# Optimization experiments

Measured on AMD Instinct MI355X. Metric: run time of the kernel, lower is better.

## Reference

```python
import jax, jax.numpy as jnp
import numpy as np

IN_C = 256
OUT_C = 256
HID = IN_C * 2
N_POINTS = 262144
N_NODES = 8192
B = 16
MAX_NODES = 512
EPS = 1e-5


def _mlp(h, w1, b1, g1, be1, w2, b2):
    # PyG MLP([C, 2C, out], norm='layer_norm'): lin -> layernorm -> relu -> (dropout, eval=identity) -> lin
    h = h @ w1 + b1
    mu = jnp.mean(h, axis=-1, keepdims=True)
    var = jnp.var(h, axis=-1, keepdims=True)
    h = (h - mu) * jax.lax.rsqrt(var + EPS) * g1 + be1
    h = jax.nn.relu(h)
    return h @ w2 + b2


def setup_inputs() -> dict:
    key = jax.random.key(0)
    ks = jax.random.split(key, 16)
    x = jax.random.normal(ks[0], (N_POINTS, IN_C), dtype=jnp.float32)
    f_point_batches = jnp.sort(jax.random.randint(ks[1], (N_POINTS,), 0, N_NODES)).astype(jnp.int32)
    # equal-sized graphs (16 graphs x 512 nodes), sorted as torch.split/pad_sequence assume
    g_node_batches = jnp.repeat(jnp.arange(B, dtype=jnp.int32), MAX_NODES)
    s = 1.0 / np.sqrt(IN_C)
    s2 = 1.0 / np.sqrt(HID)
    def lin(k, fan_in, shape, scale):
        return jax.random.uniform(k, shape, jnp.float32, -scale, scale)
    params = {}
    for i, name in enumerate(['Wq', 'Wk']):
        base = 2 + i * 6
        params[f'{name}_w1'] = lin(ks[base + 0], IN_C, (IN_C, HID), s)
        params[f'{name}_b1'] = lin(ks[base + 1], IN_C, (HID,), s)
        params[f'{name}_g1'] = jnp.ones((HID,), jnp.float32)
        params[f'{name}_be1'] = jnp.zeros((HID,), jnp.float32)
        params[f'{name}_w2'] = lin(ks[base + 2], HID, (HID, OUT_C), s2)
        params[f'{name}_b2'] = lin(ks[base + 3], HID, (OUT_C,), s2)
    return dict(x=x, f_point_batches=f_point_batches, g_node_batches=g_node_batches,
                num_graphs=B, max_nodes=MAX_NODES, **params)


def reference(x, f_point_batches, g_node_batches, num_graphs, max_nodes,
              Wq_w1, Wq_b1, Wq_g1, Wq_be1, Wq_w2, Wq_b2,
              Wk_w1, Wk_b1, Wk_g1, Wk_be1, Wk_w2, Wk_b2):
    n_nodes = g_node_batches.shape[0]
    C = x.shape[1]
    # scatter_mean over points -> per-node feature means [n_nodes, C]
    sums = jax.ops.segment_sum(x, f_point_batches, num_segments=n_nodes)
    cnt = jax.ops.segment_sum(jnp.ones((x.shape[0],), x.dtype), f_point_batches, num_segments=n_nodes)
    mean = sums / jnp.maximum(cnt, 1.0)[:, None]
    # ragged split by graph + pad_sequence -> [B, max_nodes, C]
    starts = jnp.searchsorted(g_node_batches, jnp.arange(num_graphs, dtype=g_node_batches.dtype))
    pos = jnp.arange(n_nodes) - starts[g_node_batches]
    padded = jnp.zeros((num_graphs, max_nodes, C), x.dtype).at[g_node_batches, pos].set(mean, mode='drop')
    q = _mlp(padded, Wq_w1, Wq_b1, Wq_g1, Wq_be1, Wq_w2, Wq_b2)  # [B, MAXN, out]
    k = _mlp(padded, Wk_w1, Wk_b1, Wk_g1, Wk_be1, Wk_w2, Wk_b2)
    return jnp.einsum('bnd,bmd->bnm', q, k)  # bmm(q, k^T)
```

## Files before the change

kernel.cpp:

```cpp
#include <hip/hip_runtime.h>
#include <hip/hip_bf16.h>

#define N_POINTS 262144
#define N_NODES  8192
#define IN_C     256
#define HID      512
#define OUT_C    256
#define NB       16
#define MAXN     512
#define EPSV     1e-5f
#define NPB      32

typedef __attribute__((ext_vector_type(8))) short short8;
typedef __attribute__((ext_vector_type(4))) float f32x4;
#define MFMA16(a, b, c) __builtin_amdgcn_mfma_f32_16x16x32_bf16((a), (b), (c), 0, 0, 0)


__global__ __launch_bounds__(256) void prelude_k(
    const int* __restrict__ fpb, int* __restrict__ starts,
    const float* __restrict__ W1q, const float* __restrict__ W1k,
    const float* __restrict__ W2q, const float* __restrict__ W2k,
    __hip_bfloat16* __restrict__ P1q, __hip_bfloat16* __restrict__ P1k,
    __hip_bfloat16* __restrict__ P2q, __hip_bfloat16* __restrict__ P2k)
{
  if (blockIdx.x < 1024) {
    const int i = blockIdx.x * 256 + threadIdx.x;
    const int cur = fpb[i];
    const int prev = (i == 0) ? -1 : fpb[i - 1];
    for (int n = prev + 1; n <= cur; ++n) starts[n] = i;
    if (i == N_POINTS - 1)
      for (int n = cur + 1; n <= N_NODES; ++n) starts[n] = N_POINTS;
    return;
  }
  const int bid = blockIdx.x - 1024;
  const int sel = bid >> 6;
  const float* W; __hip_bfloat16* P; int N;
  switch (sel) {
    case 0:  W = W1q; P = P1q; N = HID;   break;
    case 1:  W = W1k; P = P1k; N = HID;   break;
    case 2:  W = W2q; P = P2q; N = OUT_C; break;
    default: W = W2k; P = P2k; N = OUT_C; break;
  }
  const int idx = (bid & 63) * 256 + threadIdx.x;
  const int NF = N >> 4;
  const int lane = idx & 63;
  const int nf = (idx >> 6) % NF;
  const int ks = idx / (64 * NF);
  const int k0 = ks * 32 + (lane >> 4) * 8;
  const int n  = nf * 16 + (lane & 15);
  __hip_bfloat16 tmp[8];
  #pragma unroll
  for (int j = 0; j < 8; ++j) tmp[j] = __float2bfloat16(W[(size_t)(k0 + j) * N + n]);
  *(uint4*)(P + (size_t)idx * 8) = *(uint4*)tmp;
}

__global__ __launch_bounds__(256) void scatter_mean_k(
    const float* __restrict__ x, const int* __restrict__ starts,
    __hip_bfloat16* __restrict__ mean)
{
  const int node = blockIdx.x;
  const int start = starts[node];
  const int end   = starts[node + 1];
  const int t  = threadIdx.x;
  const int c4 = t & 63;
  const int rr = t >> 6;

  float4 s0 = make_float4(0.f, 0.f, 0.f, 0.f);
  float4 s1 = make_float4(0.f, 0.f, 0.f, 0.f);
  int r = start + rr;
  for (; r + 8 <= end; r += 8) {
    float4 v0 = *(const float4*)(x + (size_t)r * IN_C + c4 * 4);
    float4 v1 = *(const float4*)(x + (size_t)(r + 4) * IN_C + c4 * 4);
    s0.x += v0.x; s0.y += v0.y; s0.z += v0.z; s0.w += v0.w;
    s1.x += v1.x; s1.y += v1.y; s1.z += v1.z; s1.w += v1.w;
  }
  for (; r < end; r += 4) {
    float4 v = *(const float4*)(x + (size_t)r * IN_C + c4 * 4);
    s0.x += v.x; s0.y += v.y; s0.z += v.z; s0.w += v.w;
  }
  s0.x += s1.x; s0.y += s1.y; s0.z += s1.z; s0.w += s1.w;

  __shared__ float4 red[256];
  red[t] = s0;
  __syncthreads();
  if (t < 64) {
    float4 a = red[t], b = red[t + 64], c = red[t + 128], d = red[t + 192];
    const int cnt = end - start;
    const float inv = cnt > 0 ? 1.0f / (float)cnt : 0.0f;
    __hip_bfloat16 o[4];
    o[0] = __float2bfloat16((a.x + b.x + c.x + d.x) * inv);
    o[1] = __float2bfloat16((a.y + b.y + c.y + d.y) * inv);
    o[2] = __float2bfloat16((a.z + b.z + c.z + d.z) * inv);
    o[3] = __float2bfloat16((a.w + b.w + c.w + d.w) * inv);
    *(uint2*)(mean + (size_t)node * IN_C + t * 4) = *(uint2*)o;
  }
}

__global__ __launch_bounds__(512, 2) void mlp_fused_k(
    const __hip_bfloat16* __restrict__ mean,
    const __hip_bfloat16* __restrict__ P1q, const __hip_bfloat16* __restrict__ P2q,
    const float* __restrict__ b1q, const float* __restrict__ g1q,
    const float* __restrict__ be1q, const float* __restrict__ b2q,
    const __hip_bfloat16* __restrict__ P1k, const __hip_bfloat16* __restrict__ P2k,
    const float* __restrict__ b1k, const float* __restrict__ g1k,
    const float* __restrict__ be1k, const float* __restrict__ b2k,
    __hip_bfloat16* __restrict__ qo, __hip_bfloat16* __restrict__ ko)
{
  const int n0 = blockIdx.x * NPB;
  const int t = threadIdx.x;
  const int w = t >> 6, l = t & 63, lg = l >> 4, lm = l & 15;
  const int h = w >> 2;
  const int c = w & 3;

  const __hip_bfloat16* P1 = h ? P1k : P1q;
  const __hip_bfloat16* P2 = h ? P2k : P2q;
  const float* b1  = h ? b1k  : b1q;
  const float* g1  = h ? g1k  : g1q;
  const float* be1 = h ? be1k : be1q;
  const float* b2  = h ? b2k  : b2q;
  __hip_bfloat16* out = h ? ko : qo;

  __shared__ __hip_bfloat16 As[NPB * 264];
  __shared__ __hip_bfloat16 Hs[2][NPB * 520];
  __shared__ float lnp[8][NPB][2];

  #pragma unroll
  for (int it = 0; it < 2; ++it) {
    const int idx = t + it * 512;
    const int r = idx >> 5, c8 = idx & 31;
    uint4 v = *(const uint4*)(mean + (size_t)(n0 + r) * IN_C + c8 * 8);
    *(uint4*)(As + r * 264 + c8 * 8) = v;
  }
  __syncthreads();

  f32x4 acc1[2][8];
  #pragma unroll
  for (int mi = 0; mi < 2; ++mi)
    #pragma unroll
    for (int nj = 0; nj < 8; ++nj)
      #pragma unroll
      for (int r = 0; r < 4; ++r) acc1[mi][nj][r] = 0.f;

  for (int ks = 0; ks < 8; ++ks) {
    short8 a0 = *(const short8*)(As + lm * 264 + ks * 32 + lg * 8);
    short8 a1 = *(const short8*)(As + (16 + lm) * 264 + ks * 32 + lg * 8);
    const __hip_bfloat16* bp = P1 + ((size_t)(ks * 32 + c * 8) * 64 + l) * 8;
    #pragma unroll
    for (int nj = 0; nj < 8; ++nj) {
      short8 b = *(const short8*)(bp + (size_t)nj * 512);
      acc1[0][nj] = MFMA16(a0, b, acc1[0][nj]);
      acc1[1][nj] = MFMA16(a1, b, acc1[1][nj]);
    }
  }

  float b1v[8], g1v[8], e1v[8];
  #pragma unroll
  for (int nj = 0; nj < 8; ++nj) {
    const int col = c * 128 + nj * 16 + lm;
    b1v[nj] = b1[col]; g1v[nj] = g1[col]; e1v[nj] = be1[col];
  }
  #pragma unroll
  for (int mi = 0; mi < 2; ++mi)
    #pragma unroll
    for (int nj = 0; nj < 8; ++nj)
      #pragma unroll
      for (int r = 0; r < 4; ++r) acc1[mi][nj][r] += b1v[nj];

  #pragma unroll
  for (int mi = 0; mi < 2; ++mi)
    #pragma unroll
    for (int r = 0; r < 4; ++r) {
      float s = 0.f, q = 0.f;
      #pragma unroll
      for (int nj = 0; nj < 8; ++nj) {
        const float v = acc1[mi][nj][r];
        s += v; q += v * v;
      }
      #pragma unroll
      for (int off = 1; off < 16; off <<= 1) {
        s += __shfl_xor(s, off);
        q += __shfl_xor(q, off);
      }
      if (lm == 0) {
        const int row = mi * 16 + lg * 4 + r;
        lnp[w][row][0] = s;
        lnp[w][row][1] = q;
      }
    }
  __syncthreads();

  #pragma unroll
  for (int mi = 0; mi < 2; ++mi)
    #pragma unroll
    for (int r = 0; r < 4; ++r) {
      const int row = mi * 16 + lg * 4 + r;
      float S = 0.f, Q = 0.f;
      #pragma unroll
      for (int w2 = 0; w2 < 4; ++w2) {
        S += lnp[h * 4 + w2][row][0];
        Q += lnp[h * 4 + w2][row][1];
      }
      const float mu = S * (1.0f / HID);
      const float rs = rsqrtf(Q * (1.0f / HID) - mu * mu + EPSV);
      #pragma unroll
      for (int nj = 0; nj < 8; ++nj) {
        const float y = (acc1[mi][nj][r] - mu) * rs * g1v[nj] + e1v[nj];
        Hs[h][row * 520 + c * 128 + nj * 16 + lm] = __float2bfloat16(fmaxf(y, 0.f));
      }
    }
  __syncthreads();

  f32x4 acc2[2][4];
  #pragma unroll
  for (int mi = 0; mi < 2; ++mi)
    #pragma unroll
    for (int nj = 0; nj < 4; ++nj)
      #pragma unroll
      for (int r = 0; r < 4; ++r) acc2[mi][nj][r] = 0.f;

  for (int ks = 0; ks < 16; ++ks) {
    short8 a0 = *(const short8*)(Hs[h] + lm * 520 + ks * 32 + lg * 8);
    short8 a1 = *(const short8*)(Hs[h] + (16 + lm) * 520 + ks * 32 + lg * 8);
    const __hip_bfloat16* bp = P2 + ((size_t)(ks * 16 + c * 4) * 64 + l) * 8;
    #pragma unroll
    for (int nj = 0; nj < 4; ++nj) {
      short8 b = *(const short8*)(bp + (size_t)nj * 512);
      acc2[0][nj] = MFMA16(a0, b, acc2[0][nj]);
      acc2[1][nj] = MFMA16(a1, b, acc2[1][nj]);
    }
  }

  float b2v[4];
  #pragma unroll
  for (int nj = 0; nj < 4; ++nj) b2v[nj] = b2[c * 64 + nj * 16 + lm];
  #pragma unroll
  for (int mi = 0; mi < 2; ++mi)
    #pragma unroll
    for (int nj = 0; nj < 4; ++nj)
      #pragma unroll
      for (int r = 0; r < 4; ++r) {
        const int row = n0 + mi * 16 + lg * 4 + r;
        const int col = c * 64 + nj * 16 + lm;
        out[(size_t)row * OUT_C + col] = __float2bfloat16(acc2[mi][nj][r] + b2v[nj]);
      }
}

__global__ __launch_bounds__(256, 4) void bmm_k(
    const __hip_bfloat16* __restrict__ q, const __hip_bfloat16* __restrict__ k,
    float* __restrict__ out)
{
  const int b  = blockIdx.z;
  const int n0 = blockIdx.x * 64;
  const int m0 = blockIdx.y * 64;
  const int t = threadIdx.x;
  const int w = t >> 6, l = t & 63, lg = l >> 4, lm = l & 15;

  const __hip_bfloat16* qb = q + ((size_t)b * MAXN + n0 + w * 16) * OUT_C;
  const __hip_bfloat16* kb = k + ((size_t)b * MAXN + m0) * OUT_C;

  f32x4 acc[4];
  #pragma unroll
  for (int nj = 0; nj < 4; ++nj)
    #pragma unroll
    for (int r = 0; r < 4; ++r) acc[nj][r] = 0.f;

  for (int ks = 0; ks < 8; ++ks) {
    short8 a = *(const short8*)(qb + (size_t)lm * OUT_C + ks * 32 + lg * 8);
    #pragma unroll
    for (int nj = 0; nj < 4; ++nj) {
      short8 bb = *(const short8*)(kb + (size_t)(nj * 16 + lm) * OUT_C + ks * 32 + lg * 8);
      acc[nj] = MFMA16(a, bb, acc[nj]);
    }
  }

  #pragma unroll
  for (int nj = 0; nj < 4; ++nj)
    #pragma unroll
    for (int r = 0; r < 4; ++r) {
      const int nrow = n0 + w * 16 + lg * 4 + r;
      const int mcol = m0 + nj * 16 + lm;
      out[((size_t)b * MAXN + nrow) * MAXN + mcol] = acc[nj][r];
    }
}

extern "C" void kernel_launch(void* const* d_in, const int* in_sizes, int n_in,
                              void* d_out, int out_size, void* d_ws, size_t ws_size,
                              hipStream_t stream)
{
  const float* x   = (const float*)d_in[0];
  const int*   fpb = (const int*)d_in[1];
  const float* Wq_w1  = (const float*)d_in[5];
  const float* Wq_b1  = (const float*)d_in[6];
  const float* Wq_g1  = (const float*)d_in[7];
  const float* Wq_be1 = (const float*)d_in[8];
  const float* Wq_w2  = (const float*)d_in[9];
  const float* Wq_b2  = (const float*)d_in[10];
  const float* Wk_w1  = (const float*)d_in[11];
  const float* Wk_b1  = (const float*)d_in[12];
  const float* Wk_g1  = (const float*)d_in[13];
  const float* Wk_be1 = (const float*)d_in[14];
  const float* Wk_w2  = (const float*)d_in[15];
  const float* Wk_b2  = (const float*)d_in[16];

  __hip_bfloat16* ws = (__hip_bfloat16*)d_ws;
  __hip_bfloat16* P1q  = ws;
  __hip_bfloat16* P1k  = P1q + 131072;
  __hip_bfloat16* P2q  = P1k + 131072;
  __hip_bfloat16* P2k  = P2q + 131072;
  __hip_bfloat16* mean = P2k + 131072;
  __hip_bfloat16* qo   = mean + 2097152;
  __hip_bfloat16* ko   = qo + 2097152;
  int* starts = (int*)(ko + 2097152);
  float* out = (float*)d_out;

  prelude_k<<<1280, 256, 0, stream>>>(fpb, starts,
      Wq_w1, Wk_w1, Wq_w2, Wk_w2, P1q, P1k, P2q, P2k);
  scatter_mean_k<<<N_NODES, 256, 0, stream>>>(x, starts, mean);
  mlp_fused_k<<<N_NODES / NPB, 512, 0, stream>>>(
      mean, P1q, P2q, Wq_b1, Wq_g1, Wq_be1, Wq_b2,
      P1k, P2k, Wk_b1, Wk_g1, Wk_be1, Wk_b2, qo, ko);
  bmm_k<<<dim3(8, 8, NB), 256, 0, stream>>>(qo, ko, out);
}
```

Baseline: 95.51 us.

## Fuse scatter-mean into MLP kernel and halve nodes per block

The per-node mean over points is now computed inside the MLP kernel, with each wave reducing two nodes directly into shared memory. This removes the separate scatter kernel, its launch, and the global round-trip of the bf16 mean buffer. Nodes per block drop from 32 to 16 to give more blocks and higher occupancy. In exchange, weight tiles are re-read from cache twice as often per node, and the point reduction has less parallelism per node.

```diff
diff --git a/kernel.cpp b/kernel.cpp
--- a/kernel.cpp
+++ b/kernel.cpp
@@ -9,7 +9,7 @@
 #define NB       16
 #define MAXN     512
 #define EPSV     1e-5f
-#define NPB      32
+#define NPB      16
 
 typedef __attribute__((ext_vector_type(8))) short short8;
 typedef __attribute__((ext_vector_type(4))) float f32x4;
@@ -54,50 +54,8 @@
   *(uint4*)(P + (size_t)idx * 8) = *(uint4*)tmp;
 }
 
-__global__ __launch_bounds__(256) void scatter_mean_k(
+__global__ __launch_bounds__(512, 4) void fused_mlp_k(
     const float* __restrict__ x, const int* __restrict__ starts,
-    __hip_bfloat16* __restrict__ mean)
-{
-  const int node = blockIdx.x;
-  const int start = starts[node];
-  const int end   = starts[node + 1];
-  const int t  = threadIdx.x;
-  const int c4 = t & 63;
-  const int rr = t >> 6;
-
-  float4 s0 = make_float4(0.f, 0.f, 0.f, 0.f);
-  float4 s1 = make_float4(0.f, 0.f, 0.f, 0.f);
-  int r = start + rr;
-  for (; r + 8 <= end; r += 8) {
-    float4 v0 = *(const float4*)(x + (size_t)r * IN_C + c4 * 4);
-    float4 v1 = *(const float4*)(x + (size_t)(r + 4) * IN_C + c4 * 4);
-    s0.x += v0.x; s0.y += v0.y; s0.z += v0.z; s0.w += v0.w;
-    s1.x += v1.x; s1.y += v1.y; s1.z += v1.z; s1.w += v1.w;
-  }
-  for (; r < end; r += 4) {
-    float4 v = *(const float4*)(x + (size_t)r * IN_C + c4 * 4);
-    s0.x += v.x; s0.y += v.y; s0.z += v.z; s0.w += v.w;
-  }
-  s0.x += s1.x; s0.y += s1.y; s0.z += s1.z; s0.w += s1.w;
-
-  __shared__ float4 red[256];
-  red[t] = s0;
-  __syncthreads();
-  if (t < 64) {
-    float4 a = red[t], b = red[t + 64], c = red[t + 128], d = red[t + 192];
-    const int cnt = end - start;
-    const float inv = cnt > 0 ? 1.0f / (float)cnt : 0.0f;
-    __hip_bfloat16 o[4];
-    o[0] = __float2bfloat16((a.x + b.x + c.x + d.x) * inv);
-    o[1] = __float2bfloat16((a.y + b.y + c.y + d.y) * inv);
-    o[2] = __float2bfloat16((a.z + b.z + c.z + d.z) * inv);
-    o[3] = __float2bfloat16((a.w + b.w + c.w + d.w) * inv);
-    *(uint2*)(mean + (size_t)node * IN_C + t * 4) = *(uint2*)o;
-  }
-}
-
-__global__ __launch_bounds__(512, 2) void mlp_fused_k(
-    const __hip_bfloat16* __restrict__ mean,
     const __hip_bfloat16* __restrict__ P1q, const __hip_bfloat16* __restrict__ P2q,
     const float* __restrict__ b1q, const float* __restrict__ g1q,
     const float* __restrict__ be1q, const float* __restrict__ b2q,
@@ -125,31 +83,55 @@
   __shared__ float lnp[8][NPB][2];
 
   #pragma unroll
-  for (int it = 0; it < 2; ++it) {
-    const int idx = t + it * 512;
-    const int r = idx >> 5, c8 = idx & 31;
-    uint4 v = *(const uint4*)(mean + (size_t)(n0 + r) * IN_C + c8 * 8);
-    *(uint4*)(As + r * 264 + c8 * 8) = v;
+  for (int i = 0; i < 2; ++i) {
+    const int nl = w * 2 + i;
+    const int node = n0 + nl;
+    const int s_ = starts[node], e_ = starts[node + 1];
+    float4 a0 = make_float4(0.f, 0.f, 0.f, 0.f);
+    float4 a1 = a0, a2 = a0, a3 = a0;
+    int r = s_;
+    for (; r + 4 <= e_; r += 4) {
+      float4 v0 = *(const float4*)(x + (size_t)(r + 0) * IN_C + l * 4);
+      float4 v1 = *(const float4*)(x + (size_t)(r + 1) * IN_C + l * 4);
+      float4 v2 = *(const float4*)(x + (size_t)(r + 2) * IN_C + l * 4);
+      float4 v3 = *(const float4*)(x + (size_t)(r + 3) * IN_C + l * 4);
+      a0.x += v0.x; a0.y += v0.y; a0.z += v0.z; a0.w += v0.w;
+      a1.x += v1.x; a1.y += v1.y; a1.z += v1.z; a1.w += v1.w;
+      a2.x += v2.x; a2.y += v2.y; a2.z += v2.z; a2.w += v2.w;
+      a3.x += v3.x; a3.y += v3.y; a3.z += v3.z; a3.w += v3.w;
+    }
+    for (; r < e_; ++r) {
+      float4 v = *(const float4*)(x + (size_t)r * IN_C + l * 4);
+      a0.x += v.x; a0.y += v.y; a0.z += v.z; a0.w += v.w;
+    }
+    a0.x += a1.x + a2.x + a3.x;
+    a0.y += a1.y + a2.y + a3.y;
+    a0.z += a1.z + a2.z + a3.z;
+    a0.w += a1.w + a2.w + a3.w;
+    const int cnt = e_ - s_;
+    const float inv = cnt > 0 ? 1.0f / (float)cnt : 0.0f;
+    __hip_bfloat16 o[4];
+    o[0] = __float2bfloat16(a0.x * inv);
+    o[1] = __float2bfloat16(a0.y * inv);
+    o[2] = __float2bfloat16(a0.z * inv);
+    o[3] = __float2bfloat16(a0.w * inv);
+    *(uint2*)(As + nl * 264 + l * 4) = *(uint2*)o;
   }
   __syncthreads();
 
-  f32x4 acc1[2][8];
-  #pragma unroll
-  for (int mi = 0; mi < 2; ++mi)
-    #pragma unroll
-    for (int nj = 0; nj < 8; ++nj)
-      #pragma unroll
-      for (int r = 0; r < 4; ++r) acc1[mi][nj][r] = 0.f;
+  f32x4 acc1[8];
+  #pragma unroll
+  for (int nj = 0; nj < 8; ++nj)
+    #pragma unroll
+    for (int r = 0; r < 4; ++r) acc1[nj][r] = 0.f;
 
   for (int ks = 0; ks < 8; ++ks) {
-    short8 a0 = *(const short8*)(As + lm * 264 + ks * 32 + lg * 8);
-    short8 a1 = *(const short8*)(As + (16 + lm) * 264 + ks * 32 + lg * 8);
+    short8 a = *(const short8*)(As + lm * 264 + ks * 32 + lg * 8);
     const __hip_bfloat16* bp = P1 + ((size_t)(ks * 32 + c * 8) * 64 + l) * 8;
     #pragma unroll
     for (int nj = 0; nj < 8; ++nj) {
       short8 b = *(const short8*)(bp + (size_t)nj * 512);
-      acc1[0][nj] = MFMA16(a0, b, acc1[0][nj]);
-      acc1[1][nj] = MFMA16(a1, b, acc1[1][nj]);
+      acc1[nj] = MFMA16(a, b, acc1[nj]);
     }
   }
 
@@ -160,73 +142,63 @@
     b1v[nj] = b1[col]; g1v[nj] = g1[col]; e1v[nj] = be1[col];
   }
   #pragma unroll
-  for (int mi = 0; mi < 2; ++mi)
-    #pragma unroll
-    for (int nj = 0; nj < 8; ++nj)
-      #pragma unroll
-      for (int r = 0; r < 4; ++r) acc1[mi][nj][r] += b1v[nj];
-
-  #pragma unroll
-  for (int mi = 0; mi < 2; ++mi)
-    #pragma unroll
-    for (int r = 0; r < 4; ++r) {
-      float s = 0.f, q = 0.f;
-      #pragma unroll
-      for (int nj = 0; nj < 8; ++nj) {
-        const float v = acc1[mi][nj][r];
-        s += v; q += v * v;
-      }
-      #pragma unroll
-      for (int off = 1; off < 16; off <<= 1) {
-        s += __shfl_xor(s, off);
-        q += __shfl_xor(q, off);
-      }
-      if (lm == 0) {
-        const int row = mi * 16 + lg * 4 + r;
-        lnp[w][row][0] = s;
-        lnp[w][row][1] = q;
-      }
-    }
+  for (int nj = 0; nj < 8; ++nj)
+    #pragma unroll
+    for (int r = 0; r < 4; ++r) acc1[nj][r] += b1v[nj];
+
+  #pragma unroll
+  for (int r = 0; r < 4; ++r) {
+    float s = 0.f, q = 0.f;
+    #pragma unroll
+    for (int nj = 0; nj < 8; ++nj) {
+      const float v = acc1[nj][r];
+      s += v; q += v * v;
+    }
+    #pragma unroll
+    for (int off = 1; off < 16; off <<= 1) {
+      s += __shfl_xor(s, off);
+      q += __shfl_xor(q, off);
+    }
+    if (lm == 0) {
+      const int row = lg * 4 + r;
+      lnp[w][row][0] = s;
+      lnp[w][row][1] = q;
+    }
+  }
   __syncthreads();
 
   #pragma unroll
-  for (int mi = 0; mi < 2; ++mi)
-    #pragma unroll
-    for (int r = 0; r < 4; ++r) {
-      const int row = mi * 16 + lg * 4 + r;
-      float S = 0.f, Q = 0.f;
-      #pragma unroll
-      for (int w2 = 0; w2 < 4; ++w2) {
-        S += lnp[h * 4 + w2][row][0];
-        Q += lnp[h * 4 + w2][row][1];
-      }
-      const float mu = S * (1.0f / HID);
-      const float rs = rsqrtf(Q * (1.0f / HID) - mu * mu + EPSV);
-      #pragma unroll
-      for (int nj = 0; nj < 8; ++nj) {
-        const float y = (acc1[mi][nj][r] - mu) * rs * g1v[nj] + e1v[nj];
-        Hs[h][row * 520 + c * 128 + nj * 16 + lm] = __float2bfloat16(fmaxf(y, 0.f));
-      }
-    }
+  for (int r = 0; r < 4; ++r) {
+    const int row = lg * 4 + r;
+    float S = 0.f, Q = 0.f;
+    #pragma unroll
+    for (int w2 = 0; w2 < 4; ++w2) {
+      S += lnp[h * 4 + w2][row][0];
+      Q += lnp[h * 4 + w2][row][1];
+    }
+    const float mu = S * (1.0f / HID);
+    const float rs = rsqrtf(Q * (1.0f / HID) - mu * mu + EPSV);
+    #pragma unroll
+    for (int nj = 0; nj < 8; ++nj) {
+      const float y = (acc1[nj][r] - mu) * rs * g1v[nj] + e1v[nj];
+      Hs[h][row * 520 + c * 128 + nj * 16 + lm] = __float2bfloat16(fmaxf(y, 0.f));
+    }
+  }
   __syncthreads();
 
-  f32x4 acc2[2][4];
-  #pragma unroll
-  for (int mi = 0; mi < 2; ++mi)
-    #pragma unroll
-    for (int nj = 0; nj < 4; ++nj)
-      #pragma unroll
-      for (int r = 0; r < 4; ++r) acc2[mi][nj][r] = 0.f;
+  f32x4 acc2[4];
+  #pragma unroll
+  for (int nj = 0; nj < 4; ++nj)
+    #pragma unroll
+    for (int r = 0; r < 4; ++r) acc2[nj][r] = 0.f;
 
   for (int ks = 0; ks < 16; ++ks) {
-    short8 a0 = *(const short8*)(Hs[h] + lm * 520 + ks * 32 + lg * 8);
-    short8 a1 = *(const short8*)(Hs[h] + (16 + lm) * 520 + ks * 32 + lg * 8);
+    short8 a = *(const short8*)(Hs[h] + lm * 520 + ks * 32 + lg * 8);
     const __hip_bfloat16* bp = P2 + ((size_t)(ks * 16 + c * 4) * 64 + l) * 8;
     #pragma unroll
     for (int nj = 0; nj < 4; ++nj) {
       short8 b = *(const short8*)(bp + (size_t)nj * 512);
-      acc2[0][nj] = MFMA16(a0, b, acc2[0][nj]);
-      acc2[1][nj] = MFMA16(a1, b, acc2[1][nj]);
+      acc2[nj] = MFMA16(a, b, acc2[nj]);
     }
   }
 
@@ -234,15 +206,13 @@
   #pragma unroll
   for (int nj = 0; nj < 4; ++nj) b2v[nj] = b2[c * 64 + nj * 16 + lm];
   #pragma unroll
-  for (int mi = 0; mi < 2; ++mi)
-    #pragma unroll
-    for (int nj = 0; nj < 4; ++nj)
-      #pragma unroll
-      for (int r = 0; r < 4; ++r) {
-        const int row = n0 + mi * 16 + lg * 4 + r;
-        const int col = c * 64 + nj * 16 + lm;
-        out[(size_t)row * OUT_C + col] = __float2bfloat16(acc2[mi][nj][r] + b2v[nj]);
-      }
+  for (int nj = 0; nj < 4; ++nj)
+    #pragma unroll
+    for (int r = 0; r < 4; ++r) {
+      const int row = n0 + lg * 4 + r;
+      const int col = c * 64 + nj * 16 + lm;
+      out[(size_t)row * OUT_C + col] = __float2bfloat16(acc2[nj][r] + b2v[nj]);
+    }
 }
 
 __global__ __launch_bounds__(256, 4) void bmm_k(
@@ -307,17 +277,15 @@
   __hip_bfloat16* P1k  = P1q + 131072;
   __hip_bfloat16* P2q  = P1k + 131072;
   __hip_bfloat16* P2k  = P2q + 131072;
-  __hip_bfloat16* mean = P2k + 131072;
-  __hip_bfloat16* qo   = mean + 2097152;
+  __hip_bfloat16* qo   = P2k + 131072;
   __hip_bfloat16* ko   = qo + 2097152;
   int* starts = (int*)(ko + 2097152);
   float* out = (float*)d_out;
 
   prelude_k<<<1280, 256, 0, stream>>>(fpb, starts,
       Wq_w1, Wk_w1, Wq_w2, Wk_w2, P1q, P1k, P2q, P2k);
-  scatter_mean_k<<<N_NODES, 256, 0, stream>>>(x, starts, mean);
-  mlp_fused_k<<<N_NODES / NPB, 512, 0, stream>>>(
-      mean, P1q, P2q, Wq_b1, Wq_g1, Wq_be1, Wq_b2,
+  fused_mlp_k<<<N_NODES / NPB, 512, 0, stream>>>(
+      x, starts, P1q, P2q, Wq_b1, Wq_g1, Wq_be1, Wq_b2,
       P1k, P2k, Wk_b1, Wk_g1, Wk_be1, Wk_b2, qo, ko);
   bmm_k<<<dim3(8, 8, NB), 256, 0, stream>>>(qo, ko, out);
 }
```

New measurement: 89.92 us. -5.9%, faster.

## Fuse scatter-mean into MLP kernel and drop the intermediate mean buffer

Applied to the files above, without the earlier changes.

The separate scatter_mean kernel is removed. Each MLP block now reduces its own 32 nodes' points straight from x into shared memory: each wave handles 4 nodes with a 6-way unrolled, predicated nontemporal load loop. This removes one kernel launch and the write and re-read of the bf16 mean buffer. The cost is that the 256 MLP blocks must now stream all of x (268MB fp32) themselves, with fewer waves in flight than the 8192-block scatter kernel had, so memory bandwidth use may drop.

```diff
diff --git a/kernel.cpp b/kernel.cpp
--- a/kernel.cpp
+++ b/kernel.cpp
@@ -13,6 +13,7 @@
 
 typedef __attribute__((ext_vector_type(8))) short short8;
 typedef __attribute__((ext_vector_type(4))) float f32x4;
+typedef __attribute__((ext_vector_type(4))) float f4v;
 #define MFMA16(a, b, c) __builtin_amdgcn_mfma_f32_16x16x32_bf16((a), (b), (c), 0, 0, 0)
 
 
@@ -54,50 +55,8 @@
   *(uint4*)(P + (size_t)idx * 8) = *(uint4*)tmp;
 }
 
-__global__ __launch_bounds__(256) void scatter_mean_k(
+__global__ __launch_bounds__(512, 2) void fused_mlp_k(
     const float* __restrict__ x, const int* __restrict__ starts,
-    __hip_bfloat16* __restrict__ mean)
-{
-  const int node = blockIdx.x;
-  const int start = starts[node];
-  const int end   = starts[node + 1];
-  const int t  = threadIdx.x;
-  const int c4 = t & 63;
-  const int rr = t >> 6;
-
-  float4 s0 = make_float4(0.f, 0.f, 0.f, 0.f);
-  float4 s1 = make_float4(0.f, 0.f, 0.f, 0.f);
-  int r = start + rr;
-  for (; r + 8 <= end; r += 8) {
-    float4 v0 = *(const float4*)(x + (size_t)r * IN_C + c4 * 4);
-    float4 v1 = *(const float4*)(x + (size_t)(r + 4) * IN_C + c4 * 4);
-    s0.x += v0.x; s0.y += v0.y; s0.z += v0.z; s0.w += v0.w;
-    s1.x += v1.x; s1.y += v1.y; s1.z += v1.z; s1.w += v1.w;
-  }
-  for (; r < end; r += 4) {
-    float4 v = *(const float4*)(x + (size_t)r * IN_C + c4 * 4);
-    s0.x += v.x; s0.y += v.y; s0.z += v.z; s0.w += v.w;
-  }
-  s0.x += s1.x; s0.y += s1.y; s0.z += s1.z; s0.w += s1.w;
-
-  __shared__ float4 red[256];
-  red[t] = s0;
-  __syncthreads();
-  if (t < 64) {
-    float4 a = red[t], b = red[t + 64], c = red[t + 128], d = red[t + 192];
-    const int cnt = end - start;
-    const float inv = cnt > 0 ? 1.0f / (float)cnt : 0.0f;
-    __hip_bfloat16 o[4];
-    o[0] = __float2bfloat16((a.x + b.x + c.x + d.x) * inv);
-    o[1] = __float2bfloat16((a.y + b.y + c.y + d.y) * inv);
-    o[2] = __float2bfloat16((a.z + b.z + c.z + d.z) * inv);
-    o[3] = __float2bfloat16((a.w + b.w + c.w + d.w) * inv);
-    *(uint2*)(mean + (size_t)node * IN_C + t * 4) = *(uint2*)o;
-  }
-}
-
-__global__ __launch_bounds__(512, 2) void mlp_fused_k(
-    const __hip_bfloat16* __restrict__ mean,
     const __hip_bfloat16* __restrict__ P1q, const __hip_bfloat16* __restrict__ P2q,
     const float* __restrict__ b1q, const float* __restrict__ g1q,
     const float* __restrict__ be1q, const float* __restrict__ b2q,
@@ -125,11 +84,40 @@
   __shared__ float lnp[8][NPB][2];
 
   #pragma unroll
-  for (int it = 0; it < 2; ++it) {
-    const int idx = t + it * 512;
-    const int r = idx >> 5, c8 = idx & 31;
-    uint4 v = *(const uint4*)(mean + (size_t)(n0 + r) * IN_C + c8 * 8);
-    *(uint4*)(As + r * 264 + c8 * 8) = v;
+  for (int i = 0; i < 4; ++i) {
+    const int nl = w * 4 + i;
+    const int node = n0 + nl;
+    const int s_ = starts[node], e_ = starts[node + 1];
+    const int cnt = e_ - s_;
+    f4v a0 = (f4v)0.f, a1 = (f4v)0.f, a2 = (f4v)0.f, a3 = (f4v)0.f, a4 = (f4v)0.f, a5 = (f4v)0.f;
+    if (cnt > 0) {
+      for (int r = s_; r < e_; r += 6) {
+        int i0 = r,     i1 = r + 1, i2 = r + 2, i3 = r + 3, i4 = r + 4, i5 = r + 5;
+        int v1ok = i1 < e_, v2ok = i2 < e_, v3ok = i3 < e_, v4ok = i4 < e_, v5ok = i5 < e_;
+        i1 = v1ok ? i1 : s_; i2 = v2ok ? i2 : s_; i3 = v3ok ? i3 : s_;
+        i4 = v4ok ? i4 : s_; i5 = v5ok ? i5 : s_;
+        f4v v0 = __builtin_nontemporal_load((const f4v*)(x + (size_t)i0 * IN_C + l * 4));
+        f4v v1 = __builtin_nontemporal_load((const f4v*)(x + (size_t)i1 * IN_C + l * 4));
+        f4v v2 = __builtin_nontemporal_load((const f4v*)(x + (size_t)i2 * IN_C + l * 4));
+        f4v v3 = __builtin_nontemporal_load((const f4v*)(x + (size_t)i3 * IN_C + l * 4));
+        f4v v4 = __builtin_nontemporal_load((const f4v*)(x + (size_t)i4 * IN_C + l * 4));
+        f4v v5 = __builtin_nontemporal_load((const f4v*)(x + (size_t)i5 * IN_C + l * 4));
+        a0 += v0;
+        a1 += v1ok ? v1 : (f4v)0.f;
+        a2 += v2ok ? v2 : (f4v)0.f;
+        a3 += v3ok ? v3 : (f4v)0.f;
+        a4 += v4ok ? v4 : (f4v)0.f;
+        a5 += v5ok ? v5 : (f4v)0.f;
+      }
+    }
+    a0 += a1 + a2 + a3 + a4 + a5;
+    const float inv = cnt > 0 ? 1.0f / (float)cnt : 0.0f;
+    __hip_bfloat16 o[4];
+    o[0] = __float2bfloat16(a0.x * inv);
+    o[1] = __float2bfloat16(a0.y * inv);
+    o[2] = __float2bfloat16(a0.z * inv);
+    o[3] = __float2bfloat16(a0.w * inv);
+    *(uint2*)(As + nl * 264 + l * 4) = *(uint2*)o;
   }
   __syncthreads();
 
@@ -307,17 +295,15 @@
   __hip_bfloat16* P1k  = P1q + 131072;
   __hip_bfloat16* P2q  = P1k + 131072;
   __hip_bfloat16* P2k  = P2q + 131072;
-  __hip_bfloat16* mean = P2k + 131072;
-  __hip_bfloat16* qo   = mean + 2097152;
+  __hip_bfloat16* qo   = P2k + 131072;
   __hip_bfloat16* ko   = qo + 2097152;
   int* starts = (int*)(ko + 2097152);
   float* out = (float*)d_out;
 
   prelude_k<<<1280, 256, 0, stream>>>(fpb, starts,
       Wq_w1, Wk_w1, Wq_w2, Wk_w2, P1q, P1k, P2q, P2k);
-  scatter_mean_k<<<N_NODES, 256, 0, stream>>>(x, starts, mean);
-  mlp_fused_k<<<N_NODES / NPB, 512, 0, stream>>>(
-      mean, P1q, P2q, Wq_b1, Wq_g1, Wq_be1, Wq_b2,
+  fused_mlp_k<<<N_NODES / NPB, 512, 0, stream>>>(
+      x, starts, P1q, P2q, Wq_b1, Wq_g1, Wq_be1, Wq_b2,
       P1k, P2k, Wk_b1, Wk_g1, Wk_be1, Wk_b2, qo, ko);
   bmm_k<<<dim3(8, 8, NB), 256, 0, stream>>>(qo, ko, out);
 }
```

Result: faster. 92.66 us (-3.0%).
